# Kernel tuning notes

Hardware: AMD Instinct MI355X
Metric: run time of the kernel (lower is better)

## Reference

```python
import jax, jax.numpy as jnp
import numpy as np

NUM_FEATURE = 512
HIDDEN = 256
NUM_CLASSES = 10
L1 = 1e-4
ALPHA = 1e-3
BATCH = 65536


def setup_inputs() -> dict:
    key = jax.random.key(0)
    k = jax.random.split(key, 6)
    x = jax.random.normal(k[0], (BATCH, NUM_FEATURE), dtype=jnp.float32)
    y = jax.random.randint(k[1], (BATCH,), 0, NUM_CLASSES, dtype=jnp.int32)
    fc0 = jax.random.normal(k[2], (NUM_FEATURE, 512), dtype=jnp.float32) / NUM_FEATURE
    fc1 = jax.random.normal(k[3], (NUM_FEATURE, 512), dtype=jnp.float32) / NUM_FEATURE
    w = jax.random.normal(k[4], (NUM_FEATURE, HIDDEN), dtype=jnp.float32) / NUM_FEATURE
    w1 = jax.random.normal(k[5], (HIDDEN, NUM_CLASSES), dtype=jnp.float32) / HIDDEN
    return {"x": x, "y": y, "fc0": fc0, "fc1": fc1, "w": w, "w1": w1}


def reference(x, y, fc0, fc1, w, w1):
    # sigmoid-gated MLP block with residual
    x1 = x @ fc0                                   # [B, 512]
    x2 = jax.nn.relu(x @ fc1)                      # [B, 512]
    x4 = x + (1.0 + jax.nn.sigmoid(x1)) * x2       # [B, 512] residual

    # head (Dropout(p=0.0) is identity)
    logits = jax.nn.relu(x4 @ w) @ w1              # [B, 10]
    pred = jnp.argmax(logits, axis=1)

    # cross-entropy (mean over batch)
    logp = jax.nn.log_softmax(logits, axis=-1)
    ce = -jnp.mean(jnp.take_along_axis(logp, y[:, None].astype(jnp.int32), axis=1))

    # L1 penalty on all weight matrices
    l1_pen = L1 * (jnp.abs(w1).sum() + jnp.abs(w).sum()
                   + jnp.abs(fc0).sum() + jnp.abs(fc1).sum())

    # per-class variance: sum_i ||mean_{y_i} - x4_i||^2, vectorized via segment sums
    counts = jax.ops.segment_sum(jnp.ones((x4.shape[0],), jnp.float32), y,
                                 num_segments=NUM_CLASSES)
    sums = jax.ops.segment_sum(x4, y, num_segments=NUM_CLASSES)   # [10, 512]
    means = sums / jnp.maximum(counts, 1.0)[:, None]
    var_loss = jnp.sum(jnp.square(means[y] - x4))

    loss = ce + l1_pen + ALPHA * var_loss
    acc = jnp.mean((pred.astype(jnp.int32) == y.astype(jnp.int32)).astype(jnp.float32))
    return (loss, acc)
```

## Files before the change

### kernel.cpp

```cpp
#include <hip/hip_runtime.h>
#include <stdint.h>

#define BATCH 65536
#define FDIM 512
#define HDIM 256
#define NC 10
#define NREP 16

typedef short short8 __attribute__((ext_vector_type(8)));
typedef float f32x4 __attribute__((ext_vector_type(4)));

#define OFF_FC0T   ((size_t)0)
#define OFF_FC1T   (OFF_FC0T + (size_t)512*512*2)
#define OFF_WT     (OFF_FC1T + (size_t)512*512*2)
#define OFF_XT     (OFF_WT   + (size_t)256*512*2)
#define OFF_X4T    (OFF_XT   + (size_t)BATCH*512*2)
#define OFF_ACC    (OFF_X4T  + (size_t)BATCH*512*2)
#define SCAL_SUMSQ 0
#define SCAL_CE    16
#define SCAL_ACC   32
#define SCAL_L1    48
#define SCAL_VAR   64
#define SCAL_N     128
#define CNT_OFF    SCAL_N
#define GSUM_OFF   (SCAL_N + NREP*16)
#define ACC_FLOATS (GSUM_OFF + NREP*5120)

#define GLL(g,l) __builtin_amdgcn_global_load_lds((const __attribute__((address_space(1))) void*)(g), (__attribute__((address_space(3))) void*)(l), 16, 0, 0)

__device__ __forceinline__ unsigned short f2b(float f){
  unsigned u = __float_as_uint(f);
  u += 0x7FFFu + ((u >> 16) & 1u);
  return (unsigned short)(u >> 16);
}
__device__ __forceinline__ float b2f(unsigned short h){
  return __uint_as_float(((unsigned)h) << 16);
}
__device__ __forceinline__ unsigned pk2b(float f0, float f1){
  unsigned u0 = __float_as_uint(f0) + 0x8000u;
  unsigned u1 = __float_as_uint(f1) + 0x8000u;
  return __builtin_amdgcn_perm(u1, u0, 0x07060302u);
}

__global__ void k_zero(float* p, int n){
  int i = blockIdx.x*blockDim.x + threadIdx.x;
  int stride = gridDim.x*blockDim.x;
  for (; i < n; i += stride) p[i] = 0.f;
}

__global__ void k_prep(const float* __restrict__ fc0, const float* __restrict__ fc1,
                       const float* __restrict__ w,   const float* __restrict__ w1,
                       unsigned short* __restrict__ fc0T, unsigned short* __restrict__ fc1T,
                       unsigned short* __restrict__ wT,   float* __restrict__ scal){
  int i = blockIdx.x*256 + threadIdx.x;
  float l1v = 0.f;
  if (i < 32768){
    int n4 = i&15, m = (i>>4)&3, C = (i>>6)&15, J = i>>10;
    int n = J*16+n4, k8 = C*4+m;
    unsigned short o[8];
    #pragma unroll
    for (int j=0;j<8;++j){ float v = fc0[(size_t)(k8*8+j)*512 + n]; o[j]=f2b(v); l1v += fabsf(v); }
    *(short8*)&fc0T[(size_t)(J*16+C)*512 + (i&63)*8] = *(short8*)o;
  } else if (i < 65536){
    int j0 = i - 32768;
    int n4 = j0&15, m = (j0>>4)&3, C = (j0>>6)&15, J = j0>>10;
    int n = J*16+n4, k8 = C*4+m;
    unsigned short o[8];
    #pragma unroll
    for (int j=0;j<8;++j){ float v = fc1[(size_t)(k8*8+j)*512 + n]; o[j]=f2b(v); l1v += fabsf(v); }
    *(short8*)&fc1T[(size_t)(J*16+C)*512 + (j0&63)*8] = *(short8*)o;
  } else if (i < 81920){
    int j0 = i - 65536;
    int n4 = j0&15, m = (j0>>4)&3, C = (j0>>6)&15, J = j0>>10;
    int n = J*16+n4, k8 = C*4+m;
    unsigned short o[8];
    #pragma unroll
    for (int j=0;j<8;++j){ float v = w[(size_t)(k8*8+j)*256 + n]; o[j]=f2b(v); l1v += fabsf(v); }
    *(short8*)&wT[(size_t)(J*16+C)*512 + (j0&63)*8] = *(short8*)o;
  } else if (i < 82240){
    int j0 = (i - 81920)*8;
    #pragma unroll
    for (int j=0;j<8;++j) l1v += fabsf(w1[j0+j]);
  }
  for (int off = 32; off; off >>= 1) l1v += __shfl_down(l1v, off);
  if ((threadIdx.x & 63) == 0 && l1v != 0.f)
    atomicAdd(&scal[SCAL_L1 + (blockIdx.x & (NREP-1))], l1v);
}

__global__ __launch_bounds__(256) void k_xcast(const float* __restrict__ x,
                                               unsigned short* __restrict__ xT){
  int I = blockIdx.x*4 + (threadIdx.x >> 6);
  int l = threadIdx.x & 63;
  int row = I*16 + (l & 15), q = l >> 4;
  const float* src = x + (size_t)row*FDIM + q*8;
  #pragma unroll
  for (int C = 0; C < 16; ++C){
    float4 v0 = *(const float4*)(src + C*32);
    float4 v1 = *(const float4*)(src + C*32 + 4);
    unsigned o[4];
    o[0] = pk2b(v0.x, v0.y); o[1] = pk2b(v0.z, v0.w);
    o[2] = pk2b(v1.x, v1.y); o[3] = pk2b(v1.z, v1.w);
    *(short8*)&xT[(((size_t)I*16 + C) << 9) + l*8] = *(short8*)o;
  }
}

__global__ __launch_bounds__(256) void k_gemm12(
    const unsigned short* __restrict__ xT,
    const unsigned short* __restrict__ fc0T,
    const unsigned short* __restrict__ fc1T,
    unsigned short* __restrict__ x4T,
    float* __restrict__ scal)
{
  __shared__ __align__(16) char lds[32768];
  unsigned short* As    = (unsigned short*)lds;
  unsigned short* Bs0   = (unsigned short*)(lds + 16384);
  unsigned short* Bs1   = (unsigned short*)(lds + 24576);
  unsigned short* trans = (unsigned short*)(lds + 16384);
  __shared__ float red[4];

  int blk = blockIdx.x;
  int xcd = blk & 7, s = blk >> 3;
  int rowblk = xcd*64 + (s >> 3);
  int colblk = s & 7;

  int t = threadIdx.x;
  int wv = t >> 6, lane = t & 63, ln = lane & 15, quad = lane >> 4;
  int wr = wv >> 1, wc = wv & 1;

  const f32x4 zv = {0.f,0.f,0.f,0.f};
  f32x4 acc1[4][2], acc2[4][2];
  #pragma unroll
  for (int rt=0;rt<4;++rt){ acc1[rt][0]=zv; acc1[rt][1]=zv; acc2[rt][0]=zv; acc2[rt][1]=zv; }

  const char* xb  = (const char*)xT;
  const char* b0b = (const char*)fc0T;
  const char* b1b = (const char*)fc1T;

  for (int kt = 0; kt < 8; ++kt){
    #pragma unroll
    for (int i = 0; i < 2; ++i)
      #pragma unroll
      for (int c = 0; c < 2; ++c){
        size_t Ig = (size_t)(rowblk*8 + wv*2 + i);
        GLL(xb + ((Ig*16 + kt*2 + c) << 10) + lane*16,
            (char*)As + (((wv*2+i)*2 + c) << 10));
      }
    {
      size_t Jg = (size_t)(colblk*4 + wv);
      const char* g0 = b0b + ((Jg*16 + kt*2) << 10) + lane*16;
      const char* g1 = b1b + ((Jg*16 + kt*2) << 10) + lane*16;
      GLL(g0,        (char*)Bs0 + ((wv*2+0) << 10));
      GLL(g0 + 1024, (char*)Bs0 + ((wv*2+1) << 10));
      GLL(g1,        (char*)Bs1 + ((wv*2+0) << 10));
      GLL(g1 + 1024, (char*)Bs1 + ((wv*2+1) << 10));
    }
    __syncthreads();
    #pragma unroll
    for (int c = 0; c < 2; ++c){
      short8 a[4];
      #pragma unroll
      for (int rt=0;rt<4;++rt)
        a[rt] = *(const short8*)&As[(((wr*4+rt)*2 + c) << 9) + lane*8];
      #pragma unroll
      for (int ct=0;ct<2;++ct){
        int jl = wc*2 + ct;
        short8 b0 = *(const short8*)&Bs0[((jl*2+c) << 9) + lane*8];
        #pragma unroll
        for (int rt=0;rt<4;++rt)
          acc1[rt][ct] = __builtin_amdgcn_mfma_f32_16x16x32_bf16(a[rt], b0, acc1[rt][ct], 0,0,0);
        short8 b1 = *(const short8*)&Bs1[((jl*2+c) << 9) + lane*8];
        #pragma unroll
        for (int rt=0;rt<4;++rt)
          acc2[rt][ct] = __builtin_amdgcn_mfma_f32_16x16x32_bf16(a[rt], b1, acc2[rt][ct], 0,0,0);
      }
    }
    __syncthreads();
  }

  #pragma unroll
  for (int i = 0; i < 2; ++i)
    #pragma unroll
    for (int c = 0; c < 2; ++c){
      size_t Ig = (size_t)(rowblk*8 + wv*2 + i);
      GLL(xb + ((Ig*16 + colblk*2 + c) << 10) + lane*16,
          (char*)As + (((wv*2+i)*2 + c) << 10));
    }
  __syncthreads();

  float sumsq = 0.f;
  #pragma unroll
  for (int rt=0;rt<4;++rt){
    #pragma unroll
    for (int ct=0;ct<2;++ct){
      int slot_hi = (ct*2 + (ln>>3)) << 4;
      int elem = ln & 7;
      #pragma unroll
      for (int r=0;r<4;++r){
        int addr = (((wr*4+rt)*2 + wc) << 9) + ((quad*4+r) | slot_hi)*8 + elem;
        float xv  = b2f(As[addr]);
        float x1v = acc1[rt][ct][r];
        float x2v = fmaxf(acc2[rt][ct][r], 0.f);
        float gate = 1.f + 1.f/(1.f + __expf(-x1v));
        float x4v = fmaf(gate, x2v, xv);
        unsigned short ub = f2b(x4v);
        float fq = b2f(ub);
        sumsq = fmaf(fq, fq, sumsq);
        trans[addr] = ub;
      }
    }
  }
  for (int off = 32; off; off >>= 1) sumsq += __shfl_down(sumsq, off);
  if (lane == 0) red[wv] = sumsq;
  __syncthreads();
  if (t == 0)
    atomicAdd(&scal[SCAL_SUMSQ + (blk & (NREP-1))], red[0]+red[1]+red[2]+red[3]);
  {
    int lt = t >> 4;
    int I_local = lt >> 1, C_local = lt & 1;
    size_t gbase = ((size_t)(rowblk*8 + I_local)*16 + colblk*2 + C_local) << 9;
    int s0 = (t & 15)*32;
    #pragma unroll
    for (int j=0;j<4;++j)
      *(short8*)&x4T[gbase + s0 + j*8] = *(const short8*)&trans[(lt << 9) + s0 + j*8];
  }
}

__global__ __launch_bounds__(256) void k_csum(const unsigned short* __restrict__ x4T,
                                              const int* __restrict__ y,
                                              float* __restrict__ gsum){
  int w = blockIdx.x*4 + (threadIdx.x >> 6);
  int l = threadIdx.x & 63;
  int C = w & 15, Ig = w >> 4;
  int rl = l & 15, q = l >> 4;
  float a[NC][8];
  #pragma unroll
  for (int c=0;c<NC;++c)
    #pragma unroll
    for (int e=0;e<8;++e) a[c][e]=0.f;
  for (int ii = 0; ii < 64; ++ii){
    int I = Ig*64 + ii;
    int yv = y[I*16 + rl];
    short8 v = *(const short8*)&x4T[(((size_t)I*16 + C) << 9) + l*8];
    float f[8];
    #pragma unroll
    for (int e=0;e<8;++e) f[e] = b2f((unsigned short)v[e]);
    #pragma unroll
    for (int c=0;c<NC;++c){
      bool m = (yv == c);
      #pragma unroll
      for (int e=0;e<8;++e) a[c][e] += m ? f[e] : 0.f;
    }
  }
  #pragma unroll
  for (int off = 1; off < 16; off <<= 1)
    #pragma unroll
    for (int c=0;c<NC;++c)
      #pragma unroll
      for (int e=0;e<8;++e) a[c][e] += __shfl_xor(a[c][e], off);
  if (rl == 0){
    int rep = Ig & (NREP-1);
    int kb = C*32 + q*8;
    #pragma unroll
    for (int c=0;c<NC;++c)
      #pragma unroll
      for (int e=0;e<8;++e)
        atomicAdd(&gsum[(size_t)rep*5120 + c*512 + kb + e], a[c][e]);
  }
}

__global__ __launch_bounds__(512) void k_gemm3(
    const unsigned short* __restrict__ x4T,
    const unsigned short* __restrict__ wT,
    unsigned short* __restrict__ h)
{
  __shared__ __align__(16) char lds[49152];
  unsigned short* As    = (unsigned short*)lds;
  unsigned short* Bs    = (unsigned short*)(lds + 16384);
  unsigned short* trans = (unsigned short*)lds;

  int blk = blockIdx.x;
  int t = threadIdx.x;
  int wv = t >> 6, lane = t & 63, ln = lane & 15, quad = lane >> 4;
  int wr = wv >> 2, wc = wv & 3;

  const f32x4 zv = {0.f,0.f,0.f,0.f};
  f32x4 acc[4][4];
  #pragma unroll
  for (int rt=0;rt<4;++rt)
    #pragma unroll
    for (int ct=0;ct<4;++ct) acc[rt][ct] = zv;

  const char* ab = (const char*)x4T;
  const char* bb = (const char*)wT;

  for (int kt = 0; kt < 8; ++kt){
    {
      size_t Ig = (size_t)(blk*8 + wv);
      GLL(ab + ((Ig*16 + kt*2 + 0) << 10) + lane*16, (char*)As + ((wv*2+0) << 10));
      GLL(ab + ((Ig*16 + kt*2 + 1) << 10) + lane*16, (char*)As + ((wv*2+1) << 10));
    }
    #pragma unroll
    for (int i = 0; i < 2; ++i)
      #pragma unroll
      for (int c = 0; c < 2; ++c){
        size_t Jg = (size_t)(wv*2 + i);
        GLL(bb + ((Jg*16 + kt*2 + c) << 10) + lane*16,
            (char*)Bs + (((wv*2+i)*2 + c) << 10));
      }
    __syncthreads();
    #pragma unroll
    for (int c = 0; c < 2; ++c){
      short8 a[4];
      #pragma unroll
      for (int rt=0;rt<4;++rt)
        a[rt] = *(const short8*)&As[(((wr*4+rt)*2 + c) << 9) + lane*8];
      #pragma unroll
      for (int ct=0;ct<4;++ct){
        short8 b = *(const short8*)&Bs[(((wc*4+ct)*2 + c) << 9) + lane*8];
        #pragma unroll
        for (int rt=0;rt<4;++rt)
          acc[rt][ct] = __builtin_amdgcn_mfma_f32_16x16x32_bf16(a[rt], b, acc[rt][ct], 0,0,0);
      }
    }
    __syncthreads();
  }

  #pragma unroll
  for (int hf = 0; hf < 2; ++hf){
    __syncthreads();
    if ((wc >> 1) == hf){
      #pragma unroll
      for (int rt=0;rt<4;++rt)
        #pragma unroll
        for (int ct=0;ct<4;++ct)
          #pragma unroll
          for (int r=0;r<4;++r){
            int row_l = wr*64 + rt*16 + quad*4 + r;
            int col_h = (wc & 1)*64 + ct*16 + ln;
            trans[row_l*136 + col_h] = f2b(fmaxf(acc[rt][ct][r], 0.f));
          }
    }
    __syncthreads();
    int row = t >> 2, cq = (t & 3)*32;
    #pragma unroll
    for (int j=0;j<4;++j){
      short8 v = *(const short8*)&trans[row*136 + cq + j*8];
      *(short8*)&h[(size_t)(blk*128+row)*HDIM + hf*128 + cq + j*8] = v;
    }
  }
}

__global__ __launch_bounds__(256) void k_head(
    const unsigned short* __restrict__ h,
    const int* __restrict__ y,
    const float* __restrict__ w1,
    float* __restrict__ scal, float* __restrict__ gcnt)
{
  __shared__ float w1s[2560];
  __shared__ float cnt[NC];
  __shared__ float redc[4], reda[4];
  int t = threadIdx.x;
  int row = blockIdx.x*256 + t;
  int rep = blockIdx.x & (NREP-1);
  for (int i=t;i<2560;i+=256) w1s[i] = w1[i];
  if (t < NC) cnt[t] = 0.f;
  __syncthreads();
  int yv = y[row];
  atomicAdd(&cnt[yv], 1.f);
  float part[NC];
  #pragma unroll
  for (int c=0;c<NC;++c) part[c]=0.f;
  for (int j8=0;j8<32;++j8){
    short8 hv8 = *(const short8*)&h[(size_t)row*HDIM + j8*8];
    #pragma unroll
    for (int jj=0;jj<8;++jj){
      float hv = b2f((unsigned short)hv8[jj]);
      #pragma unroll
      for (int c=0;c<NC;++c) part[c] = fmaf(hv, w1s[(j8*8+jj)*10 + c], part[c]);
    }
  }
  float best = part[0]; int bi = 0;
  #pragma unroll
  for (int c=1;c<NC;++c){ if (part[c] > best){ best = part[c]; bi = c; } }
  float se = 0.f;
  #pragma unroll
  for (int c=0;c<NC;++c) se += __expf(part[c] - best);
  float lse = best + __logf(se);
  float py = part[0];
  #pragma unroll
  for (int c=1;c<NC;++c) py = (yv == c) ? part[c] : py;
  float ce = lse - py;
  float ac = (bi == yv) ? 1.f : 0.f;
  for (int off = 32; off; off >>= 1){ ce += __shfl_down(ce, off); ac += __shfl_down(ac, off); }
  int lane = t & 63, wvv = t >> 6;
  if (lane == 0){ redc[wvv] = ce; reda[wvv] = ac; }
  __syncthreads();
  if (t == 0){
    atomicAdd(&scal[SCAL_CE  + rep], redc[0]+redc[1]+redc[2]+redc[3]);
    atomicAdd(&scal[SCAL_ACC + rep], reda[0]+reda[1]+reda[2]+reda[3]);
  }
  if (t < NC) atomicAdd(&gcnt[rep*16 + t], cnt[t]);
}

__global__ void k_reduce(const float* __restrict__ gsum, const float* __restrict__ gcnt,
                         float* __restrict__ scal){
  int idx = blockIdx.x*256 + threadIdx.x;
  float S = 0.f;
  for (int r = 0; r < NREP; ++r) S += gsum[(size_t)r*5120 + idx];
  int c = idx >> 9;
  float cntv = 0.f;
  for (int r = 0; r < NREP; ++r) cntv += gcnt[r*16 + c];
  float contrib = S*S / fmaxf(cntv, 1.f);
  for (int off = 32; off; off >>= 1) contrib += __shfl_down(contrib, off);
  __shared__ float red[4];
  if ((threadIdx.x & 63) == 0) red[threadIdx.x >> 6] = contrib;
  __syncthreads();
  if (threadIdx.x == 0) atomicAdd(&scal[SCAL_VAR], red[0]+red[1]+red[2]+red[3]);
}

__global__ void k_final(const float* __restrict__ scal, float* __restrict__ out){
  if (threadIdx.x == 0 && blockIdx.x == 0){
    float sumsq=0.f, ce=0.f, acc=0.f, l1=0.f;
    for (int r=0;r<NREP;++r){
      sumsq += scal[SCAL_SUMSQ+r];
      ce    += scal[SCAL_CE+r];
      acc   += scal[SCAL_ACC+r];
      l1    += scal[SCAL_L1+r];
    }
    float var_loss = sumsq - scal[SCAL_VAR];
    float loss = ce/(float)BATCH + 1e-4f*l1 + 1e-3f*var_loss;
    out[0] = loss;
    out[1] = acc/(float)BATCH;
  }
}

extern "C" void kernel_launch(void* const* d_in, const int* in_sizes, int n_in,
                              void* d_out, int out_size, void* d_ws, size_t ws_size,
                              hipStream_t stream){
  (void)in_sizes; (void)n_in; (void)out_size; (void)ws_size;
  const float* x   = (const float*)d_in[0];
  const int*   y   = (const int*)d_in[1];
  const float* fc0 = (const float*)d_in[2];
  const float* fc1 = (const float*)d_in[3];
  const float* w   = (const float*)d_in[4];
  const float* w1  = (const float*)d_in[5];
  char* ws = (char*)d_ws;
  unsigned short* fc0T = (unsigned short*)(ws + OFF_FC0T);
  unsigned short* fc1T = (unsigned short*)(ws + OFF_FC1T);
  unsigned short* wT   = (unsigned short*)(ws + OFF_WT);
  unsigned short* xT   = (unsigned short*)(ws + OFF_XT);
  unsigned short* x4T  = (unsigned short*)(ws + OFF_X4T);
  unsigned short* h    = (unsigned short*)(ws + OFF_XT);
  float* accb = (float*)(ws + OFF_ACC);
  float* scal = accb;
  float* gcnt = accb + CNT_OFF;
  float* gsum = accb + GSUM_OFF;

  k_zero<<<161, 512, 0, stream>>>(accb, ACC_FLOATS);
  k_prep<<<322, 256, 0, stream>>>(fc0, fc1, w, w1, fc0T, fc1T, wT, scal);
  k_xcast<<<1024, 256, 0, stream>>>(x, xT);
  k_gemm12<<<4096, 256, 0, stream>>>(xT, fc0T, fc1T, x4T, scal);
  k_csum<<<256, 256, 0, stream>>>(x4T, y, gsum);
  k_gemm3<<<512, 512, 0, stream>>>(x4T, wT, h);
  k_head<<<256, 256, 0, stream>>>(h, y, w1, scal, gcnt);
  k_reduce<<<20, 256, 0, stream>>>(gsum, gcnt, scal);
  k_final<<<1, 64, 0, stream>>>(scal, (float*)d_out);
}
```

Baseline: 435.2 us.

## Fuse class-sum into GEMM12 epilogue and head into GEMM3, merge setup kernels

The zeroing, weight prep/cast and x cast kernels are merged into one setup kernel. Per-class column sums and counts move into the fc0/fc1 GEMM epilogue through LDS atomics. The head's logits, cross-entropy and accuracy are computed inside the third GEMM with an MFMA against a pre-laid-out bf16 w1, and the reduction moves into the final kernel. This removes the separate csum pass over x4, the round trip of h through global memory, and several launches. The cost is extra LDS atomics in the GEMM epilogue. The same setup launch both zeroes the accumulator buffer and atomically adds the L1 partials into it, so the L1 term can be lost if the zeroing blocks run after the adds.

```diff
diff --git a/kernel.cpp b/kernel.cpp
--- a/kernel.cpp
+++ b/kernel.cpp
@@ -20,11 +20,11 @@
 #define SCAL_CE    16
 #define SCAL_ACC   32
 #define SCAL_L1    48
-#define SCAL_VAR   64
 #define SCAL_N     128
 #define CNT_OFF    SCAL_N
 #define GSUM_OFF   (SCAL_N + NREP*16)
 #define ACC_FLOATS (GSUM_OFF + NREP*5120)
+#define OFF_W1T    (OFF_ACC + (size_t)ACC_FLOATS*4)
 
 #define GLL(g,l) __builtin_amdgcn_global_load_lds((const __attribute__((address_space(1))) void*)(g), (__attribute__((address_space(3))) void*)(l), 16, 0, 0)
 
@@ -42,65 +42,77 @@
   return __builtin_amdgcn_perm(u1, u0, 0x07060302u);
 }
 
-__global__ void k_zero(float* p, int n){
-  int i = blockIdx.x*blockDim.x + threadIdx.x;
-  int stride = gridDim.x*blockDim.x;
-  for (; i < n; i += stride) p[i] = 0.f;
-}
-
-__global__ void k_prep(const float* __restrict__ fc0, const float* __restrict__ fc1,
-                       const float* __restrict__ w,   const float* __restrict__ w1,
-                       unsigned short* __restrict__ fc0T, unsigned short* __restrict__ fc1T,
-                       unsigned short* __restrict__ wT,   float* __restrict__ scal){
-  int i = blockIdx.x*256 + threadIdx.x;
-  float l1v = 0.f;
-  if (i < 32768){
-    int n4 = i&15, m = (i>>4)&3, C = (i>>6)&15, J = i>>10;
-    int n = J*16+n4, k8 = C*4+m;
-    unsigned short o[8];
-    #pragma unroll
-    for (int j=0;j<8;++j){ float v = fc0[(size_t)(k8*8+j)*512 + n]; o[j]=f2b(v); l1v += fabsf(v); }
-    *(short8*)&fc0T[(size_t)(J*16+C)*512 + (i&63)*8] = *(short8*)o;
-  } else if (i < 65536){
-    int j0 = i - 32768;
-    int n4 = j0&15, m = (j0>>4)&3, C = (j0>>6)&15, J = j0>>10;
-    int n = J*16+n4, k8 = C*4+m;
-    unsigned short o[8];
-    #pragma unroll
-    for (int j=0;j<8;++j){ float v = fc1[(size_t)(k8*8+j)*512 + n]; o[j]=f2b(v); l1v += fabsf(v); }
-    *(short8*)&fc1T[(size_t)(J*16+C)*512 + (j0&63)*8] = *(short8*)o;
-  } else if (i < 81920){
-    int j0 = i - 65536;
-    int n4 = j0&15, m = (j0>>4)&3, C = (j0>>6)&15, J = j0>>10;
-    int n = J*16+n4, k8 = C*4+m;
-    unsigned short o[8];
-    #pragma unroll
-    for (int j=0;j<8;++j){ float v = w[(size_t)(k8*8+j)*256 + n]; o[j]=f2b(v); l1v += fabsf(v); }
-    *(short8*)&wT[(size_t)(J*16+C)*512 + (j0&63)*8] = *(short8*)o;
-  } else if (i < 82240){
-    int j0 = (i - 81920)*8;
-    #pragma unroll
-    for (int j=0;j<8;++j) l1v += fabsf(w1[j0+j]);
-  }
-  for (int off = 32; off; off >>= 1) l1v += __shfl_down(l1v, off);
-  if ((threadIdx.x & 63) == 0 && l1v != 0.f)
-    atomicAdd(&scal[SCAL_L1 + (blockIdx.x & (NREP-1))], l1v);
-}
-
-__global__ __launch_bounds__(256) void k_xcast(const float* __restrict__ x,
-                                               unsigned short* __restrict__ xT){
-  int I = blockIdx.x*4 + (threadIdx.x >> 6);
-  int l = threadIdx.x & 63;
-  int row = I*16 + (l & 15), q = l >> 4;
-  const float* src = x + (size_t)row*FDIM + q*8;
-  #pragma unroll
-  for (int C = 0; C < 16; ++C){
-    float4 v0 = *(const float4*)(src + C*32);
-    float4 v1 = *(const float4*)(src + C*32 + 4);
-    unsigned o[4];
-    o[0] = pk2b(v0.x, v0.y); o[1] = pk2b(v0.z, v0.w);
-    o[2] = pk2b(v1.x, v1.y); o[3] = pk2b(v1.z, v1.w);
-    *(short8*)&xT[(((size_t)I*16 + C) << 9) + l*8] = *(short8*)o;
+__global__ __launch_bounds__(256) void k_setup(
+    const float* __restrict__ x,   const float* __restrict__ fc0,
+    const float* __restrict__ fc1, const float* __restrict__ w,
+    const float* __restrict__ w1,
+    unsigned short* __restrict__ xT,   unsigned short* __restrict__ fc0T,
+    unsigned short* __restrict__ fc1T, unsigned short* __restrict__ wT,
+    unsigned short* __restrict__ w1T,  float* __restrict__ accb)
+{
+  int blk = blockIdx.x, t = threadIdx.x;
+  if (blk < 1024){
+    int I = blk*4 + (t >> 6);
+    int l = t & 63;
+    int row = I*16 + (l & 15), q = l >> 4;
+    const float* src = x + (size_t)row*FDIM + q*8;
+    #pragma unroll
+    for (int C = 0; C < 16; ++C){
+      float4 v0 = *(const float4*)(src + C*32);
+      float4 v1 = *(const float4*)(src + C*32 + 4);
+      unsigned o[4];
+      o[0] = pk2b(v0.x, v0.y); o[1] = pk2b(v0.z, v0.w);
+      o[2] = pk2b(v1.x, v1.y); o[3] = pk2b(v1.z, v1.w);
+      *(short8*)&xT[(((size_t)I*16 + C) << 9) + l*8] = *(short8*)o;
+    }
+    return;
+  }
+  if (blk < 1360){
+    int i = (blk - 1024)*256 + t;
+    float l1v = 0.f;
+    if (i < 32768){
+      int n4 = i&15, m = (i>>4)&3, C = (i>>6)&15, J = i>>10;
+      int n = J*16+n4, k8 = C*4+m;
+      unsigned short o[8];
+      #pragma unroll
+      for (int j=0;j<8;++j){ float v = fc0[(size_t)(k8*8+j)*512 + n]; o[j]=f2b(v); l1v += fabsf(v); }
+      *(short8*)&fc0T[(size_t)(J*16+C)*512 + (i&63)*8] = *(short8*)o;
+    } else if (i < 65536){
+      int j0 = i - 32768;
+      int n4 = j0&15, m = (j0>>4)&3, C = (j0>>6)&15, J = j0>>10;
+      int n = J*16+n4, k8 = C*4+m;
+      unsigned short o[8];
+      #pragma unroll
+      for (int j=0;j<8;++j){ float v = fc1[(size_t)(k8*8+j)*512 + n]; o[j]=f2b(v); l1v += fabsf(v); }
+      *(short8*)&fc1T[(size_t)(J*16+C)*512 + (j0&63)*8] = *(short8*)o;
+    } else if (i < 81920){
+      int j0 = i - 65536;
+      int n4 = j0&15, m = (j0>>4)&3, C = (j0>>6)&15, J = j0>>10;
+      int n = J*16+n4, k8 = C*4+m;
+      unsigned short o[8];
+      #pragma unroll
+      for (int j=0;j<8;++j){ float v = w[(size_t)(k8*8+j)*256 + n]; o[j]=f2b(v); l1v += fabsf(v); }
+      *(short8*)&wT[(size_t)(J*16+C)*512 + (j0&63)*8] = *(short8*)o;
+    } else if (i < 86016){
+      int j0 = i - 81920;
+      int C = j0 >> 9, l = (j0 >> 3) & 63, e = j0 & 7;
+      int n = l & 15, k = C*32 + (l>>4)*8 + e;
+      float v = (n < NC) ? w1[k*NC + n] : 0.f;
+      w1T[C*512 + l*8 + e] = f2b(v);
+      if (n < NC) l1v = fabsf(v);
+    }
+    for (int off = 32; off; off >>= 1) l1v += __shfl_down(l1v, off);
+    if ((t & 63) == 0 && l1v != 0.f)
+      atomicAdd(&accb[SCAL_L1 + (blk & (NREP-1))], l1v);
+    return;
+  }
+  {
+    int base = (blk - 1360)*1024;
+    #pragma unroll
+    for (int j=0;j<4;++j){
+      int idx = base + j*256 + t;
+      if (idx < ACC_FLOATS) accb[idx] = 0.f;
+    }
   }
 }
 
@@ -108,8 +120,9 @@
     const unsigned short* __restrict__ xT,
     const unsigned short* __restrict__ fc0T,
     const unsigned short* __restrict__ fc1T,
+    const int* __restrict__ y,
     unsigned short* __restrict__ x4T,
-    float* __restrict__ scal)
+    float* __restrict__ scal, float* __restrict__ gcnt, float* __restrict__ gsum)
 {
   __shared__ __align__(16) char lds[32768];
   unsigned short* As    = (unsigned short*)lds;
@@ -117,15 +130,23 @@
   unsigned short* Bs1   = (unsigned short*)(lds + 24576);
   unsigned short* trans = (unsigned short*)(lds + 16384);
   __shared__ float red[4];
+  __shared__ float csLDS[NC*64];
+  __shared__ int   ysS[128];
+  __shared__ float cntS[NC];
 
   int blk = blockIdx.x;
   int xcd = blk & 7, s = blk >> 3;
   int rowblk = xcd*64 + (s >> 3);
   int colblk = s & 7;
+  int rep = (blk ^ (blk >> 6)) & (NREP-1);
 
   int t = threadIdx.x;
   int wv = t >> 6, lane = t & 63, ln = lane & 15, quad = lane >> 4;
   int wr = wv >> 1, wc = wv & 1;
+
+  if (t < 128) ysS[t] = y[rowblk*128 + t];
+  if (t < NC) cntS[t] = 0.f;
+  for (int i = t; i < NC*64; i += 256) csLDS[i] = 0.f;
 
   const f32x4 zv = {0.f,0.f,0.f,0.f};
   f32x4 acc1[4][2], acc2[4][2];
@@ -185,18 +206,21 @@
       GLL(xb + ((Ig*16 + colblk*2 + c) << 10) + lane*16,
           (char*)As + (((wv*2+i)*2 + c) << 10));
     }
+  if (colblk == 0 && t < 128) atomicAdd(&cntS[ysS[t]], 1.f);
   __syncthreads();
 
   float sumsq = 0.f;
   #pragma unroll
   for (int rt=0;rt<4;++rt){
     #pragma unroll
-    for (int ct=0;ct<2;++ct){
-      int slot_hi = (ct*2 + (ln>>3)) << 4;
-      int elem = ln & 7;
-      #pragma unroll
-      for (int r=0;r<4;++r){
-        int addr = (((wr*4+rt)*2 + wc) << 9) + ((quad*4+r) | slot_hi)*8 + elem;
+    for (int r=0;r<4;++r){
+      int row_l = wr*64 + rt*16 + quad*4 + r;
+      int cls = ysS[row_l];
+      #pragma unroll
+      for (int ct=0;ct<2;++ct){
+        int col_l = wc*32 + ct*16 + ln;
+        int slot_hi = (ct*2 + (ln>>3)) << 4;
+        int addr = (((wr*4+rt)*2 + wc) << 9) + ((quad*4+r) | slot_hi)*8 + (ln & 7);
         float xv  = b2f(As[addr]);
         float x1v = acc1[rt][ct][r];
         float x2v = fmaxf(acc2[rt][ct][r], 0.f);
@@ -206,6 +230,7 @@
         float fq = b2f(ub);
         sumsq = fmaf(fq, fq, sumsq);
         trans[addr] = ub;
+        atomicAdd(&csLDS[cls*64 + col_l], fq);
       }
     }
   }
@@ -213,7 +238,12 @@
   if (lane == 0) red[wv] = sumsq;
   __syncthreads();
   if (t == 0)
-    atomicAdd(&scal[SCAL_SUMSQ + (blk & (NREP-1))], red[0]+red[1]+red[2]+red[3]);
+    atomicAdd(&scal[SCAL_SUMSQ + rep], red[0]+red[1]+red[2]+red[3]);
+  for (int i = t; i < NC*64; i += 256){
+    int c = i >> 6, col = i & 63;
+    atomicAdd(&gsum[(size_t)rep*5120 + c*512 + colblk*64 + col], csLDS[i]);
+  }
+  if (colblk == 0 && t < NC) atomicAdd(&gcnt[rep*16 + t], cntS[t]);
   {
     int lt = t >> 4;
     int I_local = lt >> 1, C_local = lt & 1;
@@ -225,63 +255,27 @@
   }
 }
 
-__global__ __launch_bounds__(256) void k_csum(const unsigned short* __restrict__ x4T,
-                                              const int* __restrict__ y,
-                                              float* __restrict__ gsum){
-  int w = blockIdx.x*4 + (threadIdx.x >> 6);
-  int l = threadIdx.x & 63;
-  int C = w & 15, Ig = w >> 4;
-  int rl = l & 15, q = l >> 4;
-  float a[NC][8];
-  #pragma unroll
-  for (int c=0;c<NC;++c)
-    #pragma unroll
-    for (int e=0;e<8;++e) a[c][e]=0.f;
-  for (int ii = 0; ii < 64; ++ii){
-    int I = Ig*64 + ii;
-    int yv = y[I*16 + rl];
-    short8 v = *(const short8*)&x4T[(((size_t)I*16 + C) << 9) + l*8];
-    float f[8];
-    #pragma unroll
-    for (int e=0;e<8;++e) f[e] = b2f((unsigned short)v[e]);
-    #pragma unroll
-    for (int c=0;c<NC;++c){
-      bool m = (yv == c);
-      #pragma unroll
-      for (int e=0;e<8;++e) a[c][e] += m ? f[e] : 0.f;
-    }
-  }
-  #pragma unroll
-  for (int off = 1; off < 16; off <<= 1)
-    #pragma unroll
-    for (int c=0;c<NC;++c)
-      #pragma unroll
-      for (int e=0;e<8;++e) a[c][e] += __shfl_xor(a[c][e], off);
-  if (rl == 0){
-    int rep = Ig & (NREP-1);
-    int kb = C*32 + q*8;
-    #pragma unroll
-    for (int c=0;c<NC;++c)
-      #pragma unroll
-      for (int e=0;e<8;++e)
-        atomicAdd(&gsum[(size_t)rep*5120 + c*512 + kb + e], a[c][e]);
-  }
-}
-
-__global__ __launch_bounds__(512) void k_gemm3(
+__global__ __launch_bounds__(512) void k_gemm3_head(
     const unsigned short* __restrict__ x4T,
     const unsigned short* __restrict__ wT,
-    unsigned short* __restrict__ h)
+    const unsigned short* __restrict__ w1T,
+    const int* __restrict__ y,
+    float* __restrict__ scal)
 {
   __shared__ __align__(16) char lds[49152];
-  unsigned short* As    = (unsigned short*)lds;
-  unsigned short* Bs    = (unsigned short*)(lds + 16384);
-  unsigned short* trans = (unsigned short*)lds;
+  unsigned short* As     = (unsigned short*)lds;
+  unsigned short* Bs     = (unsigned short*)(lds + 16384);
+  unsigned short* transH = (unsigned short*)lds;
+  __shared__ __align__(16) unsigned short w1s[4096];
+  __shared__ float redc[8], reda[8];
 
   int blk = blockIdx.x;
   int t = threadIdx.x;
   int wv = t >> 6, lane = t & 63, ln = lane & 15, quad = lane >> 4;
   int wr = wv >> 2, wc = wv & 3;
+  int rep = (blk ^ (blk >> 4)) & (NREP-1);
+
+  *(short8*)&w1s[t*8] = *(const short8*)&w1T[t*8];
 
   const f32x4 zv = {0.f,0.f,0.f,0.f};
   f32x4 acc[4][4];
@@ -325,6 +319,7 @@
     __syncthreads();
   }
 
+  f32x4 alog = zv;
   #pragma unroll
   for (int hf = 0; hf < 2; ++hf){
     __syncthreads();
@@ -336,100 +331,86 @@
           #pragma unroll
           for (int r=0;r<4;++r){
             int row_l = wr*64 + rt*16 + quad*4 + r;
-            int col_h = (wc & 1)*64 + ct*16 + ln;
-            trans[row_l*136 + col_h] = f2b(fmaxf(acc[rt][ct][r], 0.f));
+            int ch = (wc & 1)*64 + ct*16 + ln;
+            int tile = ((row_l >> 4) << 2) | (ch >> 5);
+            int slot = (row_l & 15) | (((ch >> 3) & 3) << 4);
+            transH[(tile << 9) + slot*8 + (ch & 7)] = f2b(fmaxf(acc[rt][ct][r], 0.f));
           }
     }
     __syncthreads();
-    int row = t >> 2, cq = (t & 3)*32;
-    #pragma unroll
-    for (int j=0;j<4;++j){
-      short8 v = *(const short8*)&trans[row*136 + cq + j*8];
-      *(short8*)&h[(size_t)(blk*128+row)*HDIM + hf*128 + cq + j*8] = v;
-    }
-  }
-}
-
-__global__ __launch_bounds__(256) void k_head(
-    const unsigned short* __restrict__ h,
-    const int* __restrict__ y,
-    const float* __restrict__ w1,
-    float* __restrict__ scal, float* __restrict__ gcnt)
-{
-  __shared__ float w1s[2560];
-  __shared__ float cnt[NC];
-  __shared__ float redc[4], reda[4];
-  int t = threadIdx.x;
-  int row = blockIdx.x*256 + t;
-  int rep = blockIdx.x & (NREP-1);
-  for (int i=t;i<2560;i+=256) w1s[i] = w1[i];
-  if (t < NC) cnt[t] = 0.f;
-  __syncthreads();
-  int yv = y[row];
-  atomicAdd(&cnt[yv], 1.f);
-  float part[NC];
-  #pragma unroll
-  for (int c=0;c<NC;++c) part[c]=0.f;
-  for (int j8=0;j8<32;++j8){
-    short8 hv8 = *(const short8*)&h[(size_t)row*HDIM + j8*8];
-    #pragma unroll
-    for (int jj=0;jj<8;++jj){
-      float hv = b2f((unsigned short)hv8[jj]);
-      #pragma unroll
-      for (int c=0;c<NC;++c) part[c] = fmaf(hv, w1s[(j8*8+jj)*10 + c], part[c]);
-    }
-  }
-  float best = part[0]; int bi = 0;
-  #pragma unroll
-  for (int c=1;c<NC;++c){ if (part[c] > best){ best = part[c]; bi = c; } }
-  float se = 0.f;
-  #pragma unroll
-  for (int c=0;c<NC;++c) se += __expf(part[c] - best);
-  float lse = best + __logf(se);
-  float py = part[0];
-  #pragma unroll
-  for (int c=1;c<NC;++c) py = (yv == c) ? part[c] : py;
-  float ce = lse - py;
-  float ac = (bi == yv) ? 1.f : 0.f;
-  for (int off = 32; off; off >>= 1){ ce += __shfl_down(ce, off); ac += __shfl_down(ac, off); }
-  int lane = t & 63, wvv = t >> 6;
-  if (lane == 0){ redc[wvv] = ce; reda[wvv] = ac; }
+    #pragma unroll
+    for (int Cl = 0; Cl < 4; ++Cl){
+      short8 a = *(const short8*)&transH[((wv*4 + Cl) << 9) + lane*8];
+      short8 b = *(const short8*)&w1s[(hf*4 + Cl)*512 + lane*8];
+      alog = __builtin_amdgcn_mfma_f32_16x16x32_bf16(a, b, alog, 0,0,0);
+    }
+  }
+
+  float ce_l = 0.f, acc_l = 0.f;
+  #pragma unroll
+  for (int r = 0; r < 4; ++r){
+    int grow = blk*128 + wv*16 + quad*4 + r;
+    int yv = y[grow];
+    float lg = (ln < NC) ? alog[r] : -1e30f;
+    float m = lg; int mi = ln;
+    #pragma unroll
+    for (int mk = 1; mk < 16; mk <<= 1){
+      float om = __shfl_xor(m, mk); int oi = __shfl_xor(mi, mk);
+      if (om > m || (om == m && oi < mi)){ m = om; mi = oi; }
+    }
+    float e  = (ln < NC) ? __expf(lg - m) : 0.f;
+    float sy = (ln == yv) ? lg : 0.f;
+    #pragma unroll
+    for (int mk = 1; mk < 16; mk <<= 1){ e += __shfl_xor(e, mk); sy += __shfl_xor(sy, mk); }
+    float lse = m + __logf(e);
+    if (ln == 0){ ce_l += (lse - sy); acc_l += (mi == yv) ? 1.f : 0.f; }
+  }
+  ce_l  += __shfl_down(ce_l, 16);  acc_l += __shfl_down(acc_l, 16);
+  ce_l  += __shfl_down(ce_l, 32);  acc_l += __shfl_down(acc_l, 32);
+  if (lane == 0){ redc[wv] = ce_l; reda[wv] = acc_l; }
   __syncthreads();
   if (t == 0){
-    atomicAdd(&scal[SCAL_CE  + rep], redc[0]+redc[1]+redc[2]+redc[3]);
-    atomicAdd(&scal[SCAL_ACC + rep], reda[0]+reda[1]+reda[2]+reda[3]);
-  }
-  if (t < NC) atomicAdd(&gcnt[rep*16 + t], cnt[t]);
-}
-
-__global__ void k_reduce(const float* __restrict__ gsum, const float* __restrict__ gcnt,
-                         float* __restrict__ scal){
-  int idx = blockIdx.x*256 + threadIdx.x;
-  float S = 0.f;
-  for (int r = 0; r < NREP; ++r) S += gsum[(size_t)r*5120 + idx];
-  int c = idx >> 9;
-  float cntv = 0.f;
-  for (int r = 0; r < NREP; ++r) cntv += gcnt[r*16 + c];
-  float contrib = S*S / fmaxf(cntv, 1.f);
+    float c = 0.f, a = 0.f;
+    #pragma unroll
+    for (int i=0;i<8;++i){ c += redc[i]; a += reda[i]; }
+    atomicAdd(&scal[SCAL_CE  + rep], c);
+    atomicAdd(&scal[SCAL_ACC + rep], a);
+  }
+}
+
+__global__ __launch_bounds__(1024) void k_final(const float* __restrict__ accb,
+                                                float* __restrict__ out){
+  const float* gsum = accb + GSUM_OFF;
+  const float* gcnt = accb + CNT_OFF;
+  int t = threadIdx.x;
+  float contrib = 0.f;
+  for (int idx = t; idx < 5120; idx += 1024){
+    float S = 0.f;
+    #pragma unroll
+    for (int r = 0; r < NREP; ++r) S += gsum[(size_t)r*5120 + idx];
+    int c = idx >> 9;
+    float cnt = 0.f;
+    #pragma unroll
+    for (int r = 0; r < NREP; ++r) cnt += gcnt[r*16 + c];
+    contrib += S*S / fmaxf(cnt, 1.f);
+  }
   for (int off = 32; off; off >>= 1) contrib += __shfl_down(contrib, off);
-  __shared__ float red[4];
-  if ((threadIdx.x & 63) == 0) red[threadIdx.x >> 6] = contrib;
+  __shared__ float red[16];
+  if ((t & 63) == 0) red[t >> 6] = contrib;
   __syncthreads();
-  if (threadIdx.x == 0) atomicAdd(&scal[SCAL_VAR], red[0]+red[1]+red[2]+red[3]);
-}
-
-__global__ void k_final(const float* __restrict__ scal, float* __restrict__ out){
-  if (threadIdx.x == 0 && blockIdx.x == 0){
+  if (t == 0){
+    float var2 = 0.f;
+    #pragma unroll
+    for (int i=0;i<16;++i) var2 += red[i];
     float sumsq=0.f, ce=0.f, acc=0.f, l1=0.f;
     for (int r=0;r<NREP;++r){
-      sumsq += scal[SCAL_SUMSQ+r];
-      ce    += scal[SCAL_CE+r];
-      acc   += scal[SCAL_ACC+r];
-      l1    += scal[SCAL_L1+r];
-    }
-    float var_loss = sumsq - scal[SCAL_VAR];
-    float loss = ce/(float)BATCH + 1e-4f*l1 + 1e-3f*var_loss;
-    out[0] = loss;
+      sumsq += accb[SCAL_SUMSQ+r];
+      ce    += accb[SCAL_CE+r];
+      acc   += accb[SCAL_ACC+r];
+      l1    += accb[SCAL_L1+r];
+    }
+    float var_loss = sumsq - var2;
+    out[0] = ce/(float)BATCH + 1e-4f*l1 + 1e-3f*var_loss;
     out[1] = acc/(float)BATCH;
   }
 }
@@ -450,19 +431,14 @@
   unsigned short* wT   = (unsigned short*)(ws + OFF_WT);
   unsigned short* xT   = (unsigned short*)(ws + OFF_XT);
   unsigned short* x4T  = (unsigned short*)(ws + OFF_X4T);
-  unsigned short* h    = (unsigned short*)(ws + OFF_XT);
+  unsigned short* w1T  = (unsigned short*)(ws + OFF_W1T);
   float* accb = (float*)(ws + OFF_ACC);
   float* scal = accb;
   float* gcnt = accb + CNT_OFF;
   float* gsum = accb + GSUM_OFF;
 
-  k_zero<<<161, 512, 0, stream>>>(accb, ACC_FLOATS);
-  k_prep<<<322, 256, 0, stream>>>(fc0, fc1, w, w1, fc0T, fc1T, wT, scal);
-  k_xcast<<<1024, 256, 0, stream>>>(x, xT);
-  k_gemm12<<<4096, 256, 0, stream>>>(xT, fc0T, fc1T, x4T, scal);
-  k_csum<<<256, 256, 0, stream>>>(x4T, y, gsum);
-  k_gemm3<<<512, 512, 0, stream>>>(x4T, wT, h);
-  k_head<<<256, 256, 0, stream>>>(h, y, w1, scal, gcnt);
-  k_reduce<<<20, 256, 0, stream>>>(gsum, gcnt, scal);
-  k_final<<<1, 64, 0, stream>>>(scal, (float*)d_out);
-}
+  k_setup<<<1441, 256, 0, stream>>>(x, fc0, fc1, w, w1, xT, fc0T, fc1T, wT, w1T, accb);
+  k_gemm12<<<4096, 256, 0, stream>>>(xT, fc0T, fc1T, y, x4T, scal, gcnt, gsum);
+  k_gemm3_head<<<512, 512, 0, stream>>>(x4T, wT, w1T, y, scal);
+  k_final<<<1, 1024, 0, stream>>>(accb, (float*)d_out);
+}
```

New measurement: 515.7 us. 1.18x slower.
